# Kernel optimization log

Hardware: AMD Instinct MI355X
Metric: run time of the kernel (lower is better)

The kernel has to match this reference:

```python
import jax, jax.numpy as jnp
import numpy as np

K, M_EMB, N_HID, D_CTX, D_ATT, M_COV = 128, 256, 256, 684, 512, 256
B, H, W = 64, 16, 48


def gru_cell(x, h, W_ih, W_hh, b_ih, b_hh):
    # PyTorch GRUCell semantics
    gi = x @ W_ih.T + b_ih
    gh = h @ W_hh.T + b_hh
    i_r, i_z, i_n = jnp.split(gi, 3, axis=-1)
    h_r, h_z, h_n = jnp.split(gh, 3, axis=-1)
    r = jax.nn.sigmoid(i_r + h_r)
    z = jax.nn.sigmoid(i_z + h_z)
    n = jnp.tanh(i_n + r * h_n)
    return (1.0 - z) * n + z * h


def setup_inputs() -> dict:
    key = jax.random.key(0)
    ks = jax.random.split(key, 24)
    s = 0.02
    inp = {
        'y': jax.random.randint(ks[0], (B,), 0, K),
        'y_mask': jnp.ones((B,), jnp.float32),
        'context': jax.random.normal(ks[1], (B, D_CTX, H, W), jnp.float32),
        'pre_hidden': jax.random.normal(ks[2], (B, N_HID), jnp.float32),
        'alpha_past': jax.random.uniform(ks[3], (B, H, W), jnp.float32),
        'emb': jax.random.normal(ks[4], (K + 1, M_EMB)) * s,
        'W_ih1': jax.random.normal(ks[5], (3 * N_HID, M_EMB)) * s,
        'W_hh1': jax.random.normal(ks[6], (3 * N_HID, N_HID)) * s,
        'b_ih1': jnp.zeros((3 * N_HID,)),
        'b_hh1': jnp.zeros((3 * N_HID,)),
        'conv_Ua_w': jax.random.normal(ks[7], (D_ATT, D_CTX, 1, 1)) * s,
        'conv_Ua_b': jnp.zeros((D_ATT,)),
        'Wa': jax.random.normal(ks[8], (D_ATT, N_HID)) * s,
        'conv_Q_w': jax.random.normal(ks[9], (M_COV, 1, 3, 3)) * s,
        'Uf': jax.random.normal(ks[10], (D_ATT, M_COV)) * s,
        'Uf_b': jnp.zeros((D_ATT,)),
        'va': jax.random.normal(ks[11], (1, D_ATT)) * s,
        'va_b': jnp.zeros((1,)),
        'W_ih2': jax.random.normal(ks[12], (3 * N_HID, D_CTX)) * s,
        'W_hh2': jax.random.normal(ks[13], (3 * N_HID, N_HID)) * s,
        'b_ih2': jnp.zeros((3 * N_HID,)),
        'b_hh2': jnp.zeros((3 * N_HID,)),
        'Wct': jax.random.normal(ks[14], (M_EMB, D_CTX)) * s,
        'Wct_b': jnp.zeros((M_EMB,)),
        'Wht': jax.random.normal(ks[15], (M_EMB, N_HID)) * s,
        'Wht_b': jnp.zeros((M_EMB,)),
        'W0': jax.random.normal(ks[16], (K, M_EMB // 2)) * s,
        'W0_b': jnp.zeros((K,)),
    }
    return inp


def reference(y, y_mask, context, pre_hidden, alpha_past, emb,
              W_ih1, W_hh1, b_ih1, b_hh1, conv_Ua_w, conv_Ua_b, Wa,
              conv_Q_w, Uf, Uf_b, va, va_b,
              W_ih2, W_hh2, b_ih2, b_hh2, Wct, Wct_b, Wht, Wht_b, W0, W0_b):
    embedded = emb[y]                                           # [B, m]
    s_hat = gru_cell(embedded, pre_hidden, W_ih1, W_hh1, b_ih1, b_hh1)
    s_hat = y_mask[:, None] * s_hat + (1.0 - y_mask)[:, None] * pre_hidden

    Wa_h1 = s_hat @ Wa.T                                        # [B, A]
    # 1x1 conv == channel projection, output in NHWC layout
    Ua_ctx = jnp.einsum('bdhw,ad->bhwa', context, conv_Ua_w[:, :, 0, 0]) + conv_Ua_b
    # 3x3 coverage conv over past attention map
    cover_F = jax.lax.conv_general_dilated(
        alpha_past[:, None, :, :], conv_Q_w, (1, 1), 'SAME',
        dimension_numbers=('NCHW', 'OIHW', 'NCHW'))              # [B, M, H, W]
    cover_F = jnp.transpose(cover_F, (0, 2, 3, 1))               # [B, H, W, M]
    cover_vector = cover_F @ Uf.T + Uf_b                         # [B, H, W, A]

    e_att = jnp.tanh(Ua_ctx + Wa_h1[:, None, None, :] + cover_vector)
    alpha = (e_att @ va.T + va_b)[..., 0].reshape(e_att.shape[0], -1)  # [B, H*W]
    alpha = jax.nn.softmax(alpha, axis=1)

    ct = jnp.einsum('bdp,bp->bd', context.reshape(context.shape[0], context.shape[1], -1), alpha)

    s = gru_cell(ct, s_hat, W_ih2, W_hh2, b_ih2, b_hh2)
    s = y_mask[:, None] * s + (1.0 - y_mask)[:, None] * s_hat

    logit = ct @ Wct.T + Wct_b + s @ Wht.T + Wht_b + embedded    # [B, m]
    logit = logit.reshape(logit.shape[0], -1, 2).max(axis=2)     # maxout -> [B, m/2]
    out = logit @ W0.T + W0_b                                    # [B, K]
    return out, s, alpha.reshape(alpha.shape[0], H, W)
```

## Files before the change

### kernel.cpp

```cpp
#include <hip/hip_runtime.h>
#include <hip/hip_bf16.h>
#include <math.h>

#define BB 64
#define KV 128
#define ME 256
#define NH 256
#define DC 684
#define DA 512
#define MC 256
#define HH_ 16
#define WW_ 48
#define HW_ 768
#define NS 22

typedef __attribute__((ext_vector_type(8))) short bf16x8;
typedef __attribute__((ext_vector_type(4))) float f32x4;

#define WS_G     0
#define WS_RB    (WS_G + 4608)
#define WS_EMB   (WS_RB + 32768)
#define WS_SH    (WS_EMB + 16384)
#define WS_AL    (WS_SH + 16384)
#define WS_CT    (WS_AL + 49152)
#define WS_APACK (WS_CT + 43776)
#define WS_GI    (WS_APACK + 180224)
#define WS_GH    (WS_GI + 49152)
#define WS_LG    WS_GI
#define WS_BP    (WS_GH + 49152)
#define WS_ALQ   (WS_BP + 17301504)
#define NEED_BYTES ((size_t)(441600 + 17301504 + 98304) * 4)

static __device__ __forceinline__ unsigned short f2b(float v) {
    __hip_bfloat16 h = __float2bfloat16(v);
    return *reinterpret_cast<unsigned short*>(&h);
}

static __device__ __forceinline__ void gl_lds16(const unsigned short* g,
                                                unsigned short* l) {
    __builtin_amdgcn_global_load_lds(
        (const __attribute__((address_space(1))) unsigned int*)g,
        (__attribute__((address_space(3))) unsigned int*)l, 16, 0, 0);
}

#define TSS 362
__global__ __launch_bounds__(512) void k_prep(
    const float* __restrict__ ctx, const float* __restrict__ Ua,
    const float* __restrict__ Uf, const float* __restrict__ convQ,
    const int* __restrict__ y, const float* __restrict__ emb,
    unsigned short* __restrict__ Bpack, unsigned short* __restrict__ Apack,
    float* __restrict__ G, float* __restrict__ embedded) {
    __shared__ unsigned short Ts[64 * TSS];
    int bx = blockIdx.x, t = threadIdx.x;
    if (bx < 768) {
        int b = bx / 12, pt = bx % 12, p0 = pt * 64;
        unsigned short* dst = Bpack + (long)(b * 12 + pt) * 22 * 2048;
        int so = t >> 8;
        int tt = t & 255;
        int pp = tt >> 2, slot = tt & 3;
        int rdoff = pp * TSS + ((slot ^ ((pp >> 1) & 3)) << 3);
        int dsub = t >> 4, q4 = (t & 15) * 4;

        for (int ch = 0; ch < 2; ch++) {
            int dbase = ch * 352;
            if (ch) __syncthreads();
#pragma unroll
            for (int iter = 0; iter < 11; iter++) {
                int d = dbase + iter * 32 + dsub;
                f32x4 v = {0.f, 0.f, 0.f, 0.f};
                if (d < DC)
                    v = *(const f32x4*)(ctx + ((long)b * DC + d) * HW_ + p0 +
                                        q4);
                int dl = d - dbase;
#pragma unroll
                for (int j = 0; j < 4; j++)
                    Ts[(q4 + j) * TSS + dl] = f2b(v[j]);
            }
            __syncthreads();
#pragma unroll
            for (int s2 = 0; s2 < 12; s2 += 2) {
                int sl = s2 + so;
                if (sl < 11) {
                    int s = ch * 11 + sl;
                    bf16x8 v = *(const bf16x8*)&Ts[rdoff + sl * 32];
                    *(bf16x8*)(dst + (long)(s * 256 + tt) * 8) = v;
                }
            }
        }
    } else if (bx < 856) {
        int bi = bx - 768;
#pragma unroll
        for (int r = 0; r < 8; r++) {
            int idx = bi * 4096 + r * 512 + t;
            int e = idx & 7, slot = (idx >> 3) & 3;
            int a = (idx >> 5) & 511, s = idx >> 14;
            int d = s * 32 + ((slot ^ ((a >> 1) & 3)) << 3) + e;
            float v = (d < DC) ? Ua[a * DC + d] : 0.f;
            Apack[idx] = f2b(v);
        }
    } else if (bx < 865) {
        int idx = (bx - 856) * 512 + t;
        if (idx < DA * 9) {
            int a = idx / 9, k = idx % 9;
            float s = 0.f;
            for (int m = 0; m < MC; m++) s += Uf[a * MC + m] * convQ[m * 9 + k];
            G[idx] = s;
        }
    } else {
        int b = bx - 865;
        if (t < ME) embedded[b * ME + t] = emb[y[b] * ME + t];
    }
}

__global__ __launch_bounds__(256) void k_G(const float* __restrict__ Uf,
                                           const float* __restrict__ convQ,
                                           float* __restrict__ G) {
    int idx = blockIdx.x * 256 + threadIdx.x;
    if (idx >= DA * 9) return;
    int a = idx / 9, k = idx % 9;
    float s = 0.f;
    for (int m = 0; m < MC; m++) s += Uf[a * MC + m] * convQ[m * 9 + k];
    G[idx] = s;
}

__global__ __launch_bounds__(256) void k_prepA(const float* __restrict__ Ua,
                                               unsigned short* __restrict__ Apack) {
    int idx = blockIdx.x * 256 + threadIdx.x;
    if (idx >= NS * DA * 32) return;
    int e = idx & 7, slot = (idx >> 3) & 3;
    int a = (idx >> 5) & 511, s = idx >> 14;
    int d = s * 32 + ((slot ^ ((a >> 1) & 3)) << 3) + e;
    float v = (d < DC) ? Ua[a * DC + d] : 0.f;
    Apack[idx] = f2b(v);
}

__global__ __launch_bounds__(256) void k_emb(const int* __restrict__ y,
                                             const float* __restrict__ emb,
                                             float* __restrict__ embedded) {
    int b = blockIdx.x, t = threadIdx.x;
    embedded[b * ME + t] = emb[y[b] * ME + t];
}

__global__ __launch_bounds__(256) void k_rows256(
    const float* __restrict__ X, const float* __restrict__ W,
    const float* __restrict__ bias, const float* __restrict__ bias2,
    float* __restrict__ out, int outStride) {
    __shared__ float Xs[64 * 257];
    __shared__ float Ws[4 * 260];
    int t = threadIdx.x, w = t >> 6, lane = t & 63;
    for (int i = t; i < 64 * 256; i += 256) {
        int bb = i >> 8, k = i & 255;
        Xs[bb * 257 + k] = X[bb * 256 + k];
    }
    int r = blockIdx.x * 4 + w;
    *(f32x4*)(Ws + w * 260 + lane * 4) = *(const f32x4*)(W + r * 256 + lane * 4);
    __syncthreads();
    const float* xrow = Xs + lane * 257;
    const float* wrow = Ws + w * 260;
    float acc = 0.f;
#pragma unroll 8
    for (int k = 0; k < 256; k++) acc += wrow[k] * xrow[k];
    acc += bias[r];
    if (bias2) acc += bias2[r];
    out[lane * outStride + r] = acc;
}

__global__ __launch_bounds__(256) void k_gih1(
    const float* __restrict__ embedded, const float* __restrict__ pre_hidden,
    const float* __restrict__ W_ih1, const float* __restrict__ W_hh1,
    const float* __restrict__ b_ih1, const float* __restrict__ b_hh1,
    float* __restrict__ gi, float* __restrict__ gh) {
    __shared__ float Xs[64 * 257];
    __shared__ float Ws[4 * 260];
    int bx = blockIdx.x, t = threadIdx.x, w = t >> 6, lane = t & 63;
    const float *X, *W, *bias;
    float* outp;
    int r;
    if (bx < 192) {
        X = embedded; W = W_ih1; bias = b_ih1; outp = gi; r = bx * 4 + w;
    } else {
        X = pre_hidden; W = W_hh1; bias = b_hh1; outp = gh; r = (bx - 192) * 4 + w;
    }
    for (int i = t; i < 64 * 256; i += 256) {
        int bb = i >> 8, k = i & 255;
        Xs[bb * 257 + k] = X[bb * 256 + k];
    }
    *(f32x4*)(Ws + w * 260 + lane * 4) = *(const f32x4*)(W + r * 256 + lane * 4);
    __syncthreads();
    const float* xrow = Xs + lane * 257;
    const float* wrow = Ws + w * 260;
    float acc = 0.f;
#pragma unroll 8
    for (int k = 0; k < 256; k++) acc += wrow[k] * xrow[k];
    outp[lane * 768 + r] = acc + bias[r];
}

__global__ __launch_bounds__(256) void k_gih2(
    const float* __restrict__ ctv, const float* __restrict__ s_hat,
    const float* __restrict__ W_ih2, const float* __restrict__ W_hh2,
    const float* __restrict__ b_ih2, const float* __restrict__ b_hh2,
    float* __restrict__ gi, float* __restrict__ gh) {
    __shared__ float Xs[64 * 257];
    __shared__ float Ws[4 * 260];
    int bx = blockIdx.x, t = threadIdx.x, w = t >> 6, lane = t & 63;
    if (bx < 192) {
        int r = bx * 4 + w;
        float acc = 0.f;
        for (int c = 0; c < 3; c++) {
            int c0 = c * 228;
            __syncthreads();
            for (int i = t; i < 64 * 228; i += 256) {
                int bb = i / 228, kk = i - bb * 228;
                Xs[bb * 229 + kk] = ctv[bb * DC + c0 + kk];
            }
            for (int j = lane; j < 228; j += 64)
                Ws[w * 260 + j] = W_ih2[r * DC + c0 + j];
            __syncthreads();
            const float* xrow = Xs + lane * 229;
            const float* wrow = Ws + w * 260;
#pragma unroll 4
            for (int k = 0; k < 228; k++) acc += wrow[k] * xrow[k];
        }
        gi[lane * 768 + r] = acc + b_ih2[r];
    } else {
        int r = (bx - 192) * 4 + w;
        for (int i = t; i < 64 * 256; i += 256) {
            int bb = i >> 8, k = i & 255;
            Xs[bb * 257 + k] = s_hat[bb * 256 + k];
        }
        *(f32x4*)(Ws + w * 260 + lane * 4) =
            *(const f32x4*)(W_hh2 + r * 256 + lane * 4);
        __syncthreads();
        const float* xrow = Xs + lane * 257;
        const float* wrow = Ws + w * 260;
        float acc = 0.f;
#pragma unroll 8
        for (int k = 0; k < 256; k++) acc += wrow[k] * xrow[k];
        gh[lane * 768 + r] = acc + b_hh2[r];
    }
}

__global__ __launch_bounds__(256) void k_gru(const float* __restrict__ gi,
                                             const float* __restrict__ gh,
                                             const float* __restrict__ h,
                                             const float* __restrict__ y_mask,
                                             float* __restrict__ outp) {
    int b = blockIdx.x, t = threadIdx.x;
    float hv = h[b * NH + t];
    float r = 1.f / (1.f + expf(-(gi[b * 768 + t] + gh[b * 768 + t])));
    float z = 1.f / (1.f + expf(-(gi[b * 768 + 256 + t] + gh[b * 768 + 256 + t])));
    float n = tanhf(gi[b * 768 + 512 + t] + r * gh[b * 768 + 512 + t]);
    float sv = (1.f - z) * n + z * hv;
    float m = y_mask[b];
    outp[b * NH + t] = m * sv + (1.f - m) * hv;
}

__global__ __launch_bounds__(512) void k_att3(
    const unsigned short* __restrict__ Apack,
    const unsigned short* __restrict__ Bpack, const float* __restrict__ G,
    const float* __restrict__ rb, const float* __restrict__ va,
    const float* __restrict__ apast, float* __restrict__ alq) {
    __shared__ __attribute__((aligned(16))) unsigned short lsA[3][8192];
    __shared__ __attribute__((aligned(16))) unsigned short lsB[3][4096];
    __shared__ float ap_s[18 * 50];
    __shared__ float part_s[8][64];
    int pt2 = blockIdx.x, ah = blockIdx.y, b = blockIdx.z;
    int t = threadIdx.x, w = t >> 6, lane = t & 63;
    int l15 = lane & 15, lg = lane >> 4;
    int aw = w & 3, pw = w >> 2;
    int sx = lg ^ ((l15 >> 1) & 3);

    for (int idx = t; idx < 900; idx += 512) {
        int hh = idx / 50, ww = idx % 50;
        float v = 0.f;
        if (hh >= 1 && hh <= HH_ && ww >= 1 && ww <= WW_)
            v = apast[b * HW_ + (hh - 1) * WW_ + (ww - 1)];
        ap_s[idx] = v;
    }
    __syncthreads();

    const unsigned short* Ap0 = Apack + ah * 8192 + w * 1024 + lane * 8;
    const unsigned short* Bp0 =
        Bpack + (long)(b * 12 + pt2 * 2 + (w >> 2)) * 22 * 2048 +
        (w & 3) * 512 + lane * 8;

#define STAGE(S, BUF)                                                        \
    do {                                                                     \
        _Pragma("unroll") for (int i_ = 0; i_ < 2; i_++)                     \
            gl_lds16(Ap0 + (long)(S)*16384 + i_ * 512,                       \
                     &lsA[BUF][w * 1024 + i_ * 512]);                        \
        gl_lds16(Bp0 + (long)(S)*2048, &lsB[BUF][w * 512]);                  \
    } while (0)

#define STEP_BODY(CUR)                                                       \
    do {                                                                     \
        const unsigned short* pA_ = &lsA[0][0] + (CUR)*8192;                 \
        const unsigned short* pB_ = &lsB[0][0] + (CUR)*4096;                 \
        bf16x8 af[4], bf[4];                                                 \
        _Pragma("unroll") for (int i = 0; i < 4; i++)                        \
            af[i] = *(const bf16x8*)&pA_[(aw * 64 + i * 16 + l15) * 32 +     \
                                         sx * 8];                            \
        _Pragma("unroll") for (int j = 0; j < 4; j++)                        \
            bf[j] = *(const bf16x8*)&pB_[pw * 2048 +                         \
                                         (j * 16 + l15) * 32 + sx * 8];     \
        _Pragma("unroll") for (int i = 0; i < 4; i++)                        \
            _Pragma("unroll") for (int j = 0; j < 4; j++)                    \
                acc[i][j] = __builtin_amdgcn_mfma_f32_16x16x32_bf16(         \
                    af[i], bf[j], acc[i][j], 0, 0, 0);                       \
    } while (0)

    f32x4 acc[4][4];
#pragma unroll
    for (int i = 0; i < 4; i++)
#pragma unroll
        for (int j = 0; j < 4; j++) acc[i][j] = {0.f, 0.f, 0.f, 0.f};

    STAGE(0, 0);
    STAGE(1, 1);

    int cur = 0;
    for (int s = 0; s < NS - 1; s++) {
        asm volatile("s_waitcnt vmcnt(3)" ::: "memory");
        __builtin_amdgcn_sched_barrier(0);
        __builtin_amdgcn_s_barrier();
        __builtin_amdgcn_sched_barrier(0);
        STEP_BODY(cur);
        if (s + 2 < NS) STAGE(s + 2, (s + 2) % 3);
        cur = (cur == 2) ? 0 : cur + 1;
    }
    asm volatile("s_waitcnt vmcnt(0)" ::: "memory");
    __builtin_amdgcn_sched_barrier(0);
    __builtin_amdgcn_s_barrier();
    __builtin_amdgcn_sched_barrier(0);
    STEP_BODY(cur);
#undef STAGE
#undef STEP_BODY

    float partial[4] = {0.f, 0.f, 0.f, 0.f};
#pragma unroll
    for (int i = 0; i < 4; i++) {
#pragma unroll
        for (int r = 0; r < 4; r++) {
            int a = ah * 256 + aw * 64 + i * 16 + lg * 4 + r;
            float rbv = rb[b * DA + a];
            float vav = va[a];
            const float* Ga = G + a * 9;
            float g0 = Ga[0], g1 = Ga[1], g2 = Ga[2], g3 = Ga[3], g4 = Ga[4];
            float g5 = Ga[5], g6 = Ga[6], g7 = Ga[7], g8 = Ga[8];
#pragma unroll
            for (int j = 0; j < 4; j++) {
                int p = pt2 * 128 + pw * 64 + j * 16 + l15;
                int hh = p / WW_, ww = p % WW_;
                const float* ap = ap_s + hh * 50 + ww;
                float cov = g0 * ap[0] + g1 * ap[1] + g2 * ap[2] +
                            g3 * ap[50] + g4 * ap[51] + g5 * ap[52] +
                            g6 * ap[100] + g7 * ap[101] + g8 * ap[102];
                float e = tanhf(acc[i][j][r] + rbv + cov);
                partial[j] += vav * e;
            }
        }
    }
#pragma unroll
    for (int j = 0; j < 4; j++) {
        partial[j] += __shfl_xor(partial[j], 16);
        partial[j] += __shfl_xor(partial[j], 32);
    }
    if (lane < 16) {
#pragma unroll
        for (int j = 0; j < 4; j++) part_s[w][j * 16 + lane] = partial[j];
    }
    __syncthreads();
    if (t < 128) {
        int pg = t >> 6, pl = t & 63;
        float sum = (part_s[pg * 4 + 0][pl] + part_s[pg * 4 + 1][pl]) +
                    (part_s[pg * 4 + 2][pl] + part_s[pg * 4 + 3][pl]);
        alq[ah * 49152 + b * HW_ + pt2 * 128 + t] = sum;
    }
}

#define LDW 40
__global__ __launch_bounds__(256) void k_att_lds(
    const unsigned short* __restrict__ Apack, const float* __restrict__ ctx,
    const float* __restrict__ G, const float* __restrict__ rb,
    const float* __restrict__ va, const float* __restrict__ apast,
    float* __restrict__ alogit) {
    __shared__ __attribute__((aligned(16))) short lsB[2][64 * LDW];
    __shared__ float ap_s[18 * 50];
    __shared__ float part_s[4 * 64];
    int b = blockIdx.y;
    int p0 = blockIdx.x * 64;
    int t = threadIdx.x;
    int w = t >> 6, lane = t & 63;
    int l15 = lane & 15, lg = lane >> 4;
    int sxA = lg ^ ((l15 >> 1) & 3);
    int pq = t & 15, kp = t >> 4;
    const float* ctx_b = ctx + (long)b * DC * HW_ + p0;

    for (int idx = t; idx < 900; idx += 256) {
        int hh = idx / 50, ww = idx % 50;
        float v = 0.f;
        if (hh >= 1 && hh <= HH_ && ww >= 1 && ww <= WW_)
            v = apast[b * HW_ + (hh - 1) * WW_ + (ww - 1)];
        ap_s[idx] = v;
    }

#define CTXLOAD(FA, FB, S)                                                   \
    do {                                                                     \
        int d_ = (S) * 32 + 2 * kp;                                          \
        const float* s0_ = ctx_b + (long)d_ * HW_ + pq;                      \
        bool g0_ = d_ < DC, g1_ = (d_ + 1) < DC;                             \
        _Pragma("unroll") for (int j_ = 0; j_ < 4; j_++) {                   \
            FA[j_] = g0_ ? s0_[16 * j_] : 0.f;                               \
            FB[j_] = g1_ ? s0_[HW_ + 16 * j_] : 0.f;                         \
        }                                                                    \
    } while (0)
#define STAGEW(FA, FB, BUF)                                                  \
    do {                                                                     \
        _Pragma("unroll") for (int j_ = 0; j_ < 4; j_++) {                   \
            ((unsigned*)lsB[BUF])[(pq + 16 * j_) * (LDW / 2) + kp] =         \
                (unsigned)f2b(FA[j_]) | ((unsigned)f2b(FB[j_]) << 16);       \
        }                                                                    \
    } while (0)
#define ALOAD(AF, S)                                                         \
    do {                                                                     \
        _Pragma("unroll") for (int i_ = 0; i_ < 8; i_++)                     \
            AF[i_] = *(const bf16x8*)(Apack +                                \
                ((long)((S)*512 + w * 128 + i_ * 16 + l15) * 4 + sxA) * 8);  \
    } while (0)
#define BREAD(BF, BUF)                                                       \
    do {                                                                     \
        _Pragma("unroll") for (int j_ = 0; j_ < 4; j_++)                     \
            BF[j_] = *(const bf16x8*)(&lsB[BUF][(j_ * 16 + l15) * LDW +      \
                                               lg * 8]);                     \
    } while (0)
#define MFMA8x4(AF, BF)                                                      \
    do {                                                                     \
        _Pragma("unroll") for (int i_ = 0; i_ < 8; i_++)                     \
            _Pragma("unroll") for (int j_ = 0; j_ < 4; j_++)                 \
                acc[i_][j_] = __builtin_amdgcn_mfma_f32_16x16x32_bf16(       \
                    AF[i_], BF[j_], acc[i_][j_], 0, 0, 0);                   \
    } while (0)

    f32x4 acc[8][4];
#pragma unroll
    for (int i = 0; i < 8; i++)
#pragma unroll
        for (int j = 0; j < 4; j++) acc[i][j] = {0.f, 0.f, 0.f, 0.f};

    float fa0[4], fb0[4], fa1[4], fb1[4];
    bf16x8 afr0[8], afr1[8], bfr[4];

    CTXLOAD(fa1, fb1, 0);
    ALOAD(afr0, 0);
    STAGEW(fa1, fb1, 0);
    CTXLOAD(fa1, fb1, 1);
    __syncthreads();

    for (int ss = 0; ss < NS; ss += 2) {
        if (ss + 2 < NS) CTXLOAD(fa0, fb0, ss + 2);
        ALOAD(afr1, ss + 1);
        BREAD(bfr, 0);
        STAGEW(fa1, fb1, 1);
        MFMA8x4(afr0, bfr);
        __syncthreads();
        if (ss + 3 < NS) CTXLOAD(fa1, fb1, ss + 3);
        if (ss + 2 < NS) {
            ALOAD(afr0, ss + 2);
            BREAD(bfr, 1);
            STAGEW(fa0, fb0, 0);
            MFMA8x4(afr1, bfr);
        } else {
            BREAD(bfr, 1);
            MFMA8x4(afr1, bfr);
        }
        __syncthreads();
    }

    float partial[4] = {0.f, 0.f, 0.f, 0.f};
#pragma unroll
    for (int i = 0; i < 8; i++) {
#pragma unroll
        for (int r = 0; r < 4; r++) {
            int a = w * 128 + i * 16 + lg * 4 + r;
            float rbv = rb[b * DA + a];
            float vav = va[a];
            const float* Ga = G + a * 9;
            float g0 = Ga[0], g1 = Ga[1], g2 = Ga[2], g3 = Ga[3], g4 = Ga[4];
            float g5 = Ga[5], g6 = Ga[6], g7 = Ga[7], g8 = Ga[8];
#pragma unroll
            for (int j = 0; j < 4; j++) {
                int p = p0 + j * 16 + l15;
                int hh = p / WW_, ww = p % WW_;
                const float* ap = ap_s + hh * 50 + ww;
                float cov = g0 * ap[0] + g1 * ap[1] + g2 * ap[2] +
                            g3 * ap[50] + g4 * ap[51] + g5 * ap[52] +
                            g6 * ap[100] + g7 * ap[101] + g8 * ap[102];
                float e = tanhf(acc[i][j][r] + rbv + cov);
                partial[j] += vav * e;
            }
        }
    }
#pragma unroll
    for (int j = 0; j < 4; j++) {
        partial[j] += __shfl_xor(partial[j], 16);
        partial[j] += __shfl_xor(partial[j], 32);
    }
    if (lane < 16) {
#pragma unroll
        for (int j = 0; j < 4; j++) part_s[w * 64 + j * 16 + lane] = partial[j];
    }
    __syncthreads();
    if (t < 64) {
        float s = part_s[t] + part_s[64 + t] + part_s[128 + t] +
                  part_s[192 + t];
        alogit[b * HW_ + p0 + t] = s;
    }
}

__global__ __launch_bounds__(256) void k_ctsm(const float* __restrict__ ctx,
                                              const float* __restrict__ alq,
                                              float* __restrict__ ct,
                                              float* __restrict__ alpha_out) {
    __shared__ float al_s[HW_];
    __shared__ float red[16];
    int b = blockIdx.y, t = threadIdx.x;
    float v[3];
    float mx = -1e30f;
    for (int i = 0; i < 3; i++) {
        int idx = b * HW_ + i * 256 + t;
        v[i] = alq[idx] + alq[49152 + idx];
        mx = fmaxf(mx, v[i]);
    }
    for (int off = 32; off > 0; off >>= 1) mx = fmaxf(mx, __shfl_down(mx, off));
    if ((t & 63) == 0) red[t >> 6] = mx;
    __syncthreads();
    if (t == 0) red[0] = fmaxf(fmaxf(red[0], red[1]), fmaxf(red[2], red[3]));
    __syncthreads();
    mx = red[0];
    float sum = 0.f;
    for (int i = 0; i < 3; i++) {
        v[i] = expf(v[i] - mx);
        sum += v[i];
    }
    for (int off = 32; off > 0; off >>= 1) sum += __shfl_down(sum, off);
    if ((t & 63) == 0) red[8 + (t >> 6)] = sum;
    __syncthreads();
    if (t == 0) red[8] = red[8] + red[9] + red[10] + red[11];
    __syncthreads();
    float inv = 1.f / red[8];
    for (int i = 0; i < 3; i++) {
        float a = v[i] * inv;
        al_s[i * 256 + t] = a;
        if (blockIdx.x == 0) alpha_out[b * HW_ + i * 256 + t] = a;
    }
    __syncthreads();
    int dc0 = blockIdx.x * 114;
    int wave = t >> 6, lane = t & 63;
    for (int d = dc0 + wave; d < dc0 + 114; d += 4) {
        const float* row = &ctx[((long)b * DC + d) * HW_];
        float s = 0.f;
#pragma unroll
        for (int q = 0; q < 12; q++) s += row[lane + q * 64] * al_s[lane + q * 64];
        for (int off = 32; off > 0; off >>= 1) s += __shfl_down(s, off);
        if (lane == 0) ct[b * DC + d] = s;
    }
}

__global__ __launch_bounds__(256) void k_logit(
    const float* __restrict__ ctv, const float* __restrict__ s,
    const float* __restrict__ embedded, const float* __restrict__ Wct,
    const float* __restrict__ Wht, const float* __restrict__ Wct_b,
    const float* __restrict__ Wht_b, float* __restrict__ lg) {
    __shared__ float Xs[64 * 257];
    __shared__ float Ws[4 * 232];
    int t = threadIdx.x, w = t >> 6, lane = t & 63;
    int r = blockIdx.x * 4 + w;
    float acc = 0.f;
    for (int c = 0; c < 3; c++) {
        int c0 = c * 228;
        __syncthreads();
        for (int i = t; i < 64 * 228; i += 256) {
            int bb = i / 228, kk = i - bb * 228;
            Xs[bb * 229 + kk] = ctv[bb * DC + c0 + kk];
        }
        for (int j = lane; j < 228; j += 64) Ws[w * 232 + j] = Wct[r * DC + c0 + j];
        __syncthreads();
        const float* xrow = Xs + lane * 229;
        const float* wrow = Ws + w * 232;
#pragma unroll 4
        for (int k = 0; k < 228; k++) acc += wrow[k] * xrow[k];
    }
    __syncthreads();
    for (int i = t; i < 64 * 256; i += 256) {
        int bb = i >> 8, k = i & 255;
        Xs[bb * 257 + k] = s[bb * 256 + k];
    }
    __syncthreads();
    const float* xrow2 = Xs + lane * 257;
    const float* wr = Wht + r * 256;
    float acc2 = 0.f;
#pragma unroll 8
    for (int k = 0; k < 256; k++) acc2 += wr[k] * xrow2[k];
    lg[lane * 256 + r] = acc + acc2 + Wct_b[r] + Wht_b[r] + embedded[lane * 256 + r];
}

__global__ __launch_bounds__(256) void k_head(const float* __restrict__ lg,
                                              const float* __restrict__ W0,
                                              const float* __restrict__ W0_b,
                                              float* __restrict__ out) {
    __shared__ float Xs[64 * 129];
    __shared__ float Ws[4 * 132];
    int t = threadIdx.x, w = t >> 6, lane = t & 63;
    for (int i = t; i < 64 * 128; i += 256) {
        int bb = i >> 7, m = i & 127;
        Xs[bb * 129 + m] = fmaxf(lg[bb * 256 + 2 * m], lg[bb * 256 + 2 * m + 1]);
    }
    int r = blockIdx.x * 4 + w;
    Ws[w * 132 + lane] = W0[r * 128 + lane];
    Ws[w * 132 + 64 + lane] = W0[r * 128 + 64 + lane];
    __syncthreads();
    const float* xrow = Xs + lane * 129;
    const float* wrow = Ws + w * 132;
    float acc = 0.f;
#pragma unroll 8
    for (int k = 0; k < 128; k++) acc += wrow[k] * xrow[k];
    out[lane * KV + r] = acc + W0_b[r];
}

extern "C" void kernel_launch(void* const* d_in, const int* in_sizes, int n_in,
                              void* d_out, int out_size, void* d_ws,
                              size_t ws_size, hipStream_t stream) {
    const int* y = (const int*)d_in[0];
    const float* y_mask = (const float*)d_in[1];
    const float* context = (const float*)d_in[2];
    const float* pre_hidden = (const float*)d_in[3];
    const float* alpha_past = (const float*)d_in[4];
    const float* emb = (const float*)d_in[5];
    const float* W_ih1 = (const float*)d_in[6];
    const float* W_hh1 = (const float*)d_in[7];
    const float* b_ih1 = (const float*)d_in[8];
    const float* b_hh1 = (const float*)d_in[9];
    const float* conv_Ua_w = (const float*)d_in[10];
    const float* conv_Ua_b = (const float*)d_in[11];
    const float* Wa = (const float*)d_in[12];
    const float* conv_Q_w = (const float*)d_in[13];
    const float* Uf = (const float*)d_in[14];
    const float* Uf_b = (const float*)d_in[15];
    const float* va = (const float*)d_in[16];
    const float* va_b = (const float*)d_in[17];
    const float* W_ih2 = (const float*)d_in[18];
    const float* W_hh2 = (const float*)d_in[19];
    const float* b_ih2 = (const float*)d_in[20];
    const float* b_hh2 = (const float*)d_in[21];
    const float* Wct = (const float*)d_in[22];
    const float* Wct_b = (const float*)d_in[23];
    const float* Wht = (const float*)d_in[24];
    const float* Wht_b = (const float*)d_in[25];
    const float* W0 = (const float*)d_in[26];
    const float* W0_b = (const float*)d_in[27];

    float* ws = (float*)d_ws;
    float* out = (float*)d_out;
    float* G = ws + WS_G;
    float* rbias = ws + WS_RB;
    float* embedded = ws + WS_EMB;
    float* s_hat = ws + WS_SH;
    float* ctv = ws + WS_CT;
    unsigned short* Apack = (unsigned short*)(ws + WS_APACK);
    float* gi = ws + WS_GI;
    float* gh = ws + WS_GH;
    float* lg = ws + WS_LG;
    unsigned short* Bpack = (unsigned short*)(ws + WS_BP);
    float* alq = ws + WS_ALQ;
    float* s_out = out + 8192;
    float* alpha_out = out + 24576;

    bool fast = ws_size >= NEED_BYTES;

    if (fast) {
        k_prep<<<dim3(929), dim3(512), 0, stream>>>(context, conv_Ua_w, Uf,
                                                    conv_Q_w, y, emb, Bpack,
                                                    Apack, G, embedded);
    } else {
        k_G<<<dim3(18), dim3(256), 0, stream>>>(Uf, conv_Q_w, G);
        k_prepA<<<dim3((NS * DA * 32 + 255) / 256), dim3(256), 0, stream>>>(
            conv_Ua_w, Apack);
        k_emb<<<dim3(64), dim3(256), 0, stream>>>(y, emb, embedded);
    }
    k_gih1<<<dim3(384), dim3(256), 0, stream>>>(embedded, pre_hidden, W_ih1,
                                                W_hh1, b_ih1, b_hh1, gi, gh);
    k_gru<<<dim3(64), dim3(256), 0, stream>>>(gi, gh, pre_hidden, y_mask, s_hat);
    k_rows256<<<dim3(128), dim3(256), 0, stream>>>(s_hat, Wa, conv_Ua_b, Uf_b,
                                                   rbias, 512);
    if (fast) {
        k_att3<<<dim3(6, 2, 64), dim3(512), 0, stream>>>(
            Apack, Bpack, G, rbias, va, alpha_past, alq);
    } else {
        hipMemsetAsync(alq + 49152, 0, (size_t)49152 * sizeof(float), stream);
        k_att_lds<<<dim3(12, 64), dim3(256), 0, stream>>>(
            Apack, context, G, rbias, va, alpha_past, alq);
    }
    k_ctsm<<<dim3(6, 64), dim3(256), 0, stream>>>(context, alq, ctv, alpha_out);
    k_gih2<<<dim3(384), dim3(256), 0, stream>>>(ctv, s_hat, W_ih2, W_hh2, b_ih2,
                                                b_hh2, gi, gh);
    k_gru<<<dim3(64), dim3(256), 0, stream>>>(gi, gh, s_hat, y_mask, s_out);
    k_logit<<<dim3(64), dim3(256), 0, stream>>>(ctv, s_out, embedded, Wct, Wht,
                                                Wct_b, Wht_b, lg);
    k_head<<<dim3(32), dim3(256), 0, stream>>>(lg, W0, W0_b, out);
}
```

Before: 227.8 us.

## Double-buffer context transpose in prep kernel and issue GEMM stage loads earlier

The context fp32-to-bf16 transpose/pack in k_prep changes from two sequential 352-channel chunks to four 192-channel chunks in a double-buffered LDS tile. Global loads for the next chunk are issued before the packed stores of the previous chunk, so load latency overlaps the LDS transpose and the writes. Separately, the attention GEMM loop now issues the prefetch STAGE for step s+2 before the MFMA body instead of after it, giving loads more time in flight. The cost is more live registers and a tighter triple-buffer reuse window, since the stage being overwritten must already be free when it is issued.

New measurement: 235.5 us. 1.03x slower.

```diff
diff --git a/kernel.cpp b/kernel.cpp
--- a/kernel.cpp
+++ b/kernel.cpp
@@ -43,14 +43,14 @@
         (__attribute__((address_space(3))) unsigned int*)l, 16, 0, 0);
 }
 
-#define TSS 362
+#define TSS2 198
 __global__ __launch_bounds__(512) void k_prep(
     const float* __restrict__ ctx, const float* __restrict__ Ua,
     const float* __restrict__ Uf, const float* __restrict__ convQ,
     const int* __restrict__ y, const float* __restrict__ emb,
     unsigned short* __restrict__ Bpack, unsigned short* __restrict__ Apack,
     float* __restrict__ G, float* __restrict__ embedded) {
-    __shared__ unsigned short Ts[64 * TSS];
+    __shared__ unsigned short Ts[2][64 * TSS2];
     int bx = blockIdx.x, t = threadIdx.x;
     if (bx < 768) {
         int b = bx / 12, pt = bx % 12, p0 = pt * 64;
@@ -58,35 +58,56 @@
         int so = t >> 8;
         int tt = t & 255;
         int pp = tt >> 2, slot = tt & 3;
-        int rdoff = pp * TSS + ((slot ^ ((pp >> 1) & 3)) << 3);
+        int rdoff = pp * TSS2 + ((slot ^ ((pp >> 1) & 3)) << 3);
         int dsub = t >> 4, q4 = (t & 15) * 4;
-
-        for (int ch = 0; ch < 2; ch++) {
-            int dbase = ch * 352;
-            if (ch) __syncthreads();
-#pragma unroll
-            for (int iter = 0; iter < 11; iter++) {
-                int d = dbase + iter * 32 + dsub;
-                f32x4 v = {0.f, 0.f, 0.f, 0.f};
-                if (d < DC)
-                    v = *(const f32x4*)(ctx + ((long)b * DC + d) * HW_ + p0 +
-                                        q4);
-                int dl = d - dbase;
-#pragma unroll
-                for (int j = 0; j < 4; j++)
-                    Ts[(q4 + j) * TSS + dl] = f2b(v[j]);
-            }
-            __syncthreads();
-#pragma unroll
-            for (int s2 = 0; s2 < 12; s2 += 2) {
-                int sl = s2 + so;
-                if (sl < 11) {
-                    int s = ch * 11 + sl;
-                    bf16x8 v = *(const bf16x8*)&Ts[rdoff + sl * 32];
-                    *(bf16x8*)(dst + (long)(s * 256 + tt) * 8) = v;
-                }
-            }
-        }
+        const float* cbase = ctx + (long)b * DC * HW_ + p0 + q4;
+
+#define P1LOAD(CB, RN, PRE)                                                  \
+        _Pragma("unroll") for (int r_ = 0; r_ < (RN); r_++) {                \
+            int d_ = (CB) + r_ * 32 + dsub;                                  \
+            PRE[r_] = (d_ < DC) ? *(const f32x4*)(cbase + (long)d_ * HW_)    \
+                                : (f32x4){0.f, 0.f, 0.f, 0.f};               \
+        }
+#define TSWRITE(BUF, RN, PRE)                                                \
+        _Pragma("unroll") for (int r_ = 0; r_ < (RN); r_++) {                \
+            int dl_ = r_ * 32 + dsub;                                        \
+            _Pragma("unroll") for (int j_ = 0; j_ < 4; j_++)                 \
+                Ts[BUF][(q4 + j_) * TSS2 + dl_] = f2b(PRE[r_][j_]);          \
+        }
+#define P2EMIT(BUF, SB, SN)                                                  \
+        _Pragma("unroll") for (int s2_ = 0; s2_ < (SN); s2_ += 2) {          \
+            int sl_ = s2_ + so;                                              \
+            bf16x8 v_ = *(const bf16x8*)&Ts[BUF][rdoff + sl_ * 32];          \
+            *(bf16x8*)(dst + (long)(((SB) + sl_) * 256 + tt) * 8) = v_;      \
+        }
+
+        f32x4 pre[6];
+        P1LOAD(0, 6, pre);
+        __builtin_amdgcn_sched_barrier(0);
+        TSWRITE(0, 6, pre);
+        __syncthreads();
+        P1LOAD(192, 6, pre);
+        __builtin_amdgcn_sched_barrier(0);
+        P2EMIT(0, 0, 6);
+        __builtin_amdgcn_sched_barrier(0);
+        TSWRITE(1, 6, pre);
+        __syncthreads();
+        P1LOAD(384, 6, pre);
+        __builtin_amdgcn_sched_barrier(0);
+        P2EMIT(1, 6, 6);
+        __builtin_amdgcn_sched_barrier(0);
+        TSWRITE(0, 6, pre);
+        __syncthreads();
+        P1LOAD(576, 4, pre);
+        __builtin_amdgcn_sched_barrier(0);
+        P2EMIT(0, 12, 6);
+        __builtin_amdgcn_sched_barrier(0);
+        TSWRITE(1, 4, pre);
+        __syncthreads();
+        P2EMIT(1, 18, 4);
+#undef P1LOAD
+#undef TSWRITE
+#undef P2EMIT
     } else if (bx < 856) {
         int bi = bx - 768;
 #pragma unroll
@@ -324,8 +345,8 @@
         __builtin_amdgcn_sched_barrier(0);
         __builtin_amdgcn_s_barrier();
         __builtin_amdgcn_sched_barrier(0);
+        if (s + 2 < NS) STAGE(s + 2, (s + 2) % 3);
         STEP_BODY(cur);
-        if (s + 2 < NS) STAGE(s + 2, (s + 2) % 3);
         cur = (cur == 2) ? 0 : cur + 1;
     }
     asm volatile("s_waitcnt vmcnt(0)" ::: "memory");
```

## Pipeline context transpose-pack with triple-buffered direct global-to-LDS loads

Applied to the files above, without the earlier changes.

Replaces the two-chunk register-load/transposed-LDS-store packing of the context tensor in k_prep with a triple-buffered pipeline that loads fp32 rows straight into LDS via global_load_lds. Each stage of 64 channels is then read transposed from LDS, converted to bf16, and written to the packed B layout. The aim is to overlap global loads with the conversion and cut register traffic and LDS bank conflicts from the strided transposed stores. The cost is LDS growth to 48KB of fp32 buffers, which may lower occupancy, and a manual vmcnt/barrier protocol whose correctness depends on exact load counts. Out-of-range rows are clamped to row 0 rather than zero-filled, so padding channels now carry nonzero values.

New measurement: 227.4 us. Within noise of the previous version (-0.2%).

```diff
diff --git a/kernel.cpp b/kernel.cpp
--- a/kernel.cpp
+++ b/kernel.cpp
@@ -36,57 +36,73 @@
     return *reinterpret_cast<unsigned short*>(&h);
 }
 
-static __device__ __forceinline__ void gl_lds16(const unsigned short* g,
-                                                unsigned short* l) {
+static __device__ __forceinline__ void gl_lds16(const void* g, void* l) {
     __builtin_amdgcn_global_load_lds(
         (const __attribute__((address_space(1))) unsigned int*)g,
         (__attribute__((address_space(3))) unsigned int*)l, 16, 0, 0);
 }
 
-#define TSS 362
 __global__ __launch_bounds__(512) void k_prep(
     const float* __restrict__ ctx, const float* __restrict__ Ua,
     const float* __restrict__ Uf, const float* __restrict__ convQ,
     const int* __restrict__ y, const float* __restrict__ emb,
     unsigned short* __restrict__ Bpack, unsigned short* __restrict__ Apack,
     float* __restrict__ G, float* __restrict__ embedded) {
-    __shared__ unsigned short Ts[64 * TSS];
+    __shared__ float lsC[3][4096];
     int bx = blockIdx.x, t = threadIdx.x;
     if (bx < 768) {
         int b = bx / 12, pt = bx % 12, p0 = pt * 64;
         unsigned short* dst = Bpack + (long)(b * 12 + pt) * 22 * 2048;
+        int w = t >> 6, lane = t & 63;
         int so = t >> 8;
         int tt = t & 255;
         int pp = tt >> 2, slot = tt & 3;
-        int rdoff = pp * TSS + ((slot ^ ((pp >> 1) & 3)) << 3);
-        int dsub = t >> 4, q4 = (t & 15) * 4;
-
-        for (int ch = 0; ch < 2; ch++) {
-            int dbase = ch * 352;
-            if (ch) __syncthreads();
-#pragma unroll
-            for (int iter = 0; iter < 11; iter++) {
-                int d = dbase + iter * 32 + dsub;
-                f32x4 v = {0.f, 0.f, 0.f, 0.f};
-                if (d < DC)
-                    v = *(const f32x4*)(ctx + ((long)b * DC + d) * HW_ + p0 +
-                                        q4);
-                int dl = d - dbase;
-#pragma unroll
-                for (int j = 0; j < 4; j++)
-                    Ts[(q4 + j) * TSS + dl] = f2b(v[j]);
-            }
-            __syncthreads();
-#pragma unroll
-            for (int s2 = 0; s2 < 12; s2 += 2) {
-                int sl = s2 + so;
-                if (sl < 11) {
-                    int s = ch * 11 + sl;
-                    bf16x8 v = *(const bf16x8*)&Ts[rdoff + sl * 32];
-                    *(bf16x8*)(dst + (long)(s * 256 + tt) * 8) = v;
-                }
-            }
-        }
+        int swz = (slot ^ ((pp >> 1) & 3)) << 3;
+        int lrow = lane >> 4, lcol = (lane & 15) * 4;
+        const float* cb = ctx + (long)b * DC * HW_ + p0 + lcol;
+
+#define STAGEP(S, BUF)                                                       \
+    do {                                                                     \
+        _Pragma("unroll") for (int i_ = 0; i_ < 2; i_++) {                   \
+            int row_ = (S)*64 + w * 8 + i_ * 4 + lrow;                       \
+            int rowc_ = (row_ < DC) ? row_ : 0;                              \
+            gl_lds16(cb + (long)rowc_ * HW_,                                 \
+                     &lsC[BUF][(w * 8 + i_ * 4) * 64]);                      \
+        }                                                                    \
+    } while (0)
+
+#define BODYP(BUF, S)                                                        \
+    do {                                                                     \
+        int dbase_ = so * 32 + swz;                                          \
+        float f_[8];                                                         \
+        _Pragma("unroll") for (int k_ = 0; k_ < 8; k_++)                     \
+            f_[k_] = lsC[BUF][(dbase_ + k_) * 64 + pp];                      \
+        bf16x8 o_;                                                           \
+        _Pragma("unroll") for (int k_ = 0; k_ < 8; k_++)                     \
+            o_[k_] = (short)f2b(f_[k_]);                                     \
+        int s_ = (S)*2 + so;                                                 \
+        *(bf16x8*)(dst + (long)(s_ * 256 + tt) * 8) = o_;                    \
+    } while (0)
+
+        STAGEP(0, 0);
+        STAGEP(1, 1);
+        int cur = 0;
+        for (int S = 0; S < 10; S++) {
+            asm volatile("s_waitcnt vmcnt(2)" ::: "memory");
+            __builtin_amdgcn_sched_barrier(0);
+            __builtin_amdgcn_s_barrier();
+            __builtin_amdgcn_sched_barrier(0);
+            BODYP(cur, S);
+            STAGEP(S + 2, (S + 2) % 3);
+            cur = (cur == 2) ? 0 : cur + 1;
+        }
+        asm volatile("s_waitcnt vmcnt(0)" ::: "memory");
+        __builtin_amdgcn_sched_barrier(0);
+        __builtin_amdgcn_s_barrier();
+        __builtin_amdgcn_sched_barrier(0);
+        BODYP(cur, 10);
+#undef STAGEP
+#undef BODYP
     } else if (bx < 856) {
         int bi = bx - 768;
 #pragma unroll
```
